# Optimization experiments

Hardware: AMD Instinct MI355X
Metric: run time of the kernel (lower is better)

## Reference

```python
import jax, jax.numpy as jnp
import numpy as np


def setup_inputs() -> dict:
    key = jax.random.key(0)
    B, T, F = 1000000, 60, 4
    inputs = jax.random.normal(key, (B, T, F), dtype=jnp.float32)
    return {"inputs": inputs, "window_size": 30, "n_forecast": 14, "target_idx": 0}


def reference(inputs, window_size, n_forecast, target_idx):
    # y: last window_size steps of the target feature -> [B, W]
    y = inputs[:, -window_size:, target_idx]
    W = window_size
    # design points x = 0..W-1 (identical for every sample)
    x = jnp.arange(W, dtype=inputs.dtype)            # [W]
    x_mean = x.mean()
    xc = x - x_mean                                  # centered x, [W]
    sxx = jnp.sum(xc * xc)                           # scalar
    y_mean = y.mean(axis=1)                          # [B]
    # closed-form simple OLS: slope = sum((x-xm)*y)/Sxx (centered y cancels)
    slope = (y @ xc) / sxx                           # [B]
    intercept = y_mean - slope * x_mean              # [B]
    # predict at future timesteps W .. W+n_forecast-1
    t_future = jnp.arange(W, W + n_forecast, dtype=inputs.dtype)  # [n_forecast]
    result = intercept[:, None] + slope[:, None] * t_future[None, :]  # [B, n_forecast]
    return result
```

## Files before the change

kernel.cpp:

```cpp
#include <hip/hip_runtime.h>


#define NBATCH 256
#define W      30
#define NF     14
#define TDIM   60

typedef const __attribute__((address_space(1))) void gvoid_t;
typedef __attribute__((address_space(3))) void lvoid_t;

__global__ __launch_bounds__(256)
void linreg_forecast_kernel(const float* __restrict__ in,
                            float4* __restrict__ out4,
                            int B, int out4_total)
{
    __shared__ __align__(16) float y[NBATCH * W];

    const int tid = threadIdx.x;
    const int B0  = blockIdx.x * NBATCH;

    #pragma unroll
    for (int k = 0; k < W; ++k) {
        int i  = tid + (k << 8);
        int bb = i / W;
        int t  = i - bb * W;
        int gb = B0 + bb;
        if (gb > B - 1) gb = B - 1;
        const float* src = in + ((size_t)(gb * TDIM + W + t) << 2);
        __builtin_amdgcn_global_load_lds((gvoid_t*)src, (lvoid_t*)&y[i], 4, 0, 0);
    }
    __syncthreads();

    float slope, intercept;
    {
        const float* row = &y[tid * W];
        float s0 = 0.f, s1 = 0.f;
        #pragma unroll
        for (int t = 0; t < W; ++t) {
            float v = row[t];
            s0 += v;
            s1 += v * ((float)t - 14.5f);
        }
        slope     = s1 * (1.0f / 2247.5f);
        intercept = s0 * (1.0f / 30.0f) - slope * 14.5f;
    }
    __syncthreads();

    {
        int gb = B0 + tid;
        if (gb < B) {
            float* r = &y[tid * NF];
            #pragma unroll
            for (int j = 0; j < NF; ++j)
                r[j] = intercept + slope * (float)(W + j);
        }
    }
    __syncthreads();

    const int base4 = blockIdx.x * (NBATCH * NF / 4);
    const float4* res4 = (const float4*)y;
    #pragma unroll
    for (int k = 0; k < 4; ++k) {
        int i = tid + (k << 8);
        if (i < NBATCH * NF / 4 && base4 + i < out4_total)
            out4[base4 + i] = res4[i];
    }
}

extern "C" void kernel_launch(void* const* d_in, const int* in_sizes, int n_in,
                              void* d_out, int out_size, void* d_ws, size_t ws_size,
                              hipStream_t stream)
{
    const float* in = (const float*)d_in[0];
    float*      out = (float*)d_out;
    int B = in_sizes[0] / (TDIM * 4);
    int grid = (B + NBATCH - 1) / NBATCH;
    linreg_forecast_kernel<<<grid, 256, 0, stream>>>(
        in, (float4*)out, B, out_size / 4);
}
```

Before: 1.135 ms.

## Map one 32-lane group per sample with shuffle reduction instead of LDS staging

Replaces the LDS-staged design, where each block loads 256 samples via global_load_lds and each thread reduces one row, with a layout that gives each sample its own 32-lane group. Each lane loads one timestep as a float4, and the two sums are reduced with xor shuffles. The LDS buffer, the block barriers and the staged output copy are all removed, and the 14 forecasts are written directly. The goal is more memory-level parallelism and less synchronisation. The cost is loading all four features per timestep, leaving 2 of every 32 lanes idle, and launching a much larger grid with less coalesced output stores.

Result: no change. 1.124 ms (-1.0%).

```diff
diff --git a/kernel.cpp b/kernel.cpp
--- a/kernel.cpp
+++ b/kernel.cpp
@@ -1,70 +1,38 @@
 #include <hip/hip_runtime.h>
 
 
-#define NBATCH 256
-#define W      30
-#define NF     14
-#define TDIM   60
-
-typedef const __attribute__((address_space(1))) void gvoid_t;
-typedef __attribute__((address_space(3))) void lvoid_t;
+#define W    30
+#define NF   14
+#define TDIM 60
+#define BPB  8
 
 __global__ __launch_bounds__(256)
-void linreg_forecast_kernel(const float* __restrict__ in,
-                            float4* __restrict__ out4,
-                            int B, int out4_total)
+void linreg_forecast_kernel(const float4* __restrict__ in4,
+                            float* __restrict__ out,
+                            int B)
 {
-    __shared__ __align__(16) float y[NBATCH * W];
+    const int tid  = threadIdx.x;
+    const int lane = tid & 31;
+    const int b    = blockIdx.x * BPB + (tid >> 5);
+    const int gb   = (b < B) ? b : (B - 1);
 
-    const int tid = threadIdx.x;
-    const int B0  = blockIdx.x * NBATCH;
+    const int t = (lane < W) ? lane : (W - 1);
+    float4 v = in4[(size_t)gb * TDIM + W + t];
+    float  y = (lane < W) ? v.x : 0.0f;
 
+    float s0 = y;
+    float s1 = y * ((float)t - 14.5f);
     #pragma unroll
-    for (int k = 0; k < W; ++k) {
-        int i  = tid + (k << 8);
-        int bb = i / W;
-        int t  = i - bb * W;
-        int gb = B0 + bb;
-        if (gb > B - 1) gb = B - 1;
-        const float* src = in + ((size_t)(gb * TDIM + W + t) << 2);
-        __builtin_amdgcn_global_load_lds((gvoid_t*)src, (lvoid_t*)&y[i], 4, 0, 0);
+    for (int m = 1; m <= 16; m <<= 1) {
+        s0 += __shfl_xor(s0, m);
+        s1 += __shfl_xor(s1, m);
     }
-    __syncthreads();
 
-    float slope, intercept;
-    {
-        const float* row = &y[tid * W];
-        float s0 = 0.f, s1 = 0.f;
-        #pragma unroll
-        for (int t = 0; t < W; ++t) {
-            float v = row[t];
-            s0 += v;
-            s1 += v * ((float)t - 14.5f);
-        }
-        slope     = s1 * (1.0f / 2247.5f);
-        intercept = s0 * (1.0f / 30.0f) - slope * 14.5f;
-    }
-    __syncthreads();
+    const float slope     = s1 * (1.0f / 2247.5f);
+    const float intercept = s0 * (1.0f / 30.0f) - slope * 14.5f;
 
-    {
-        int gb = B0 + tid;
-        if (gb < B) {
-            float* r = &y[tid * NF];
-            #pragma unroll
-            for (int j = 0; j < NF; ++j)
-                r[j] = intercept + slope * (float)(W + j);
-        }
-    }
-    __syncthreads();
-
-    const int base4 = blockIdx.x * (NBATCH * NF / 4);
-    const float4* res4 = (const float4*)y;
-    #pragma unroll
-    for (int k = 0; k < 4; ++k) {
-        int i = tid + (k << 8);
-        if (i < NBATCH * NF / 4 && base4 + i < out4_total)
-            out4[base4 + i] = res4[i];
-    }
+    if (lane < NF && b < B)
+        out[b * NF + lane] = intercept + slope * (float)(W + lane);
 }
 
 extern "C" void kernel_launch(void* const* d_in, const int* in_sizes, int n_in,
@@ -74,7 +42,7 @@
     const float* in = (const float*)d_in[0];
     float*      out = (float*)d_out;
     int B = in_sizes[0] / (TDIM * 4);
-    int grid = (B + NBATCH - 1) / NBATCH;
+    int grid = (B + BPB - 1) / BPB;
     linreg_forecast_kernel<<<grid, 256, 0, stream>>>(
-        in, (float4*)out, B, out_size / 4);
+        (const float4*)in, out, B);
 }
```
